# Optimization experiments

Measured on AMD Instinct MI355X. Metric: run time of the kernel, lower is better.

Reference implementation:

```python
import jax, jax.numpy as jnp
import numpy as np

N, D, H, E = 50000, 64, 4, 400000
LN_EPS = 1e-5


def setup_inputs() -> dict:
    key = jax.random.key(0)
    ks = jax.random.split(key, 8)
    x = jax.random.normal(ks[0], (N, D), dtype=jnp.float32)
    edge_index = jax.random.randint(ks[1], (2, E), 0, N, dtype=jnp.int64)
    # nn.Linear(dim, dim*heads, bias=False): weight shape (H*D, D)
    W_lin = jax.random.normal(ks[2], (H * D, D), dtype=jnp.float32) * (1.0 / np.sqrt(D))
    attn_src = jax.random.normal(ks[3], (H, D), dtype=jnp.float32) * 0.1
    attn_dst = jax.random.normal(ks[4], (H, D), dtype=jnp.float32) * 0.1
    # nn.Linear(dim*heads, dim): weight (D, H*D), bias (D,)
    W_out = jax.random.normal(ks[5], (D, H * D), dtype=jnp.float32) * (1.0 / np.sqrt(H * D))
    b_out = jnp.zeros((D,), dtype=jnp.float32)
    ln_g = jnp.ones((D,), dtype=jnp.float32)
    ln_b = jnp.zeros((D,), dtype=jnp.float32)
    return {"x": x, "edge_index": edge_index, "W_lin": W_lin,
            "attn_src": attn_src, "attn_dst": attn_dst,
            "W_out": W_out, "b_out": b_out, "ln_g": ln_g, "ln_b": ln_b}


def reference(x, edge_index, W_lin, attn_src, attn_dst, W_out, b_out, ln_g, ln_b):
    n = x.shape[0]
    i, j = edge_index[0], edge_index[1]  # dst, src node ids per edge
    xh = (x @ W_lin.T).reshape(n, H, D)                 # [N,H,D]
    # per-node attention contributions (equivalent to per-edge dot in source)
    s_dst = jnp.einsum('nhd,hd->nh', xh, attn_dst)      # [N,H]
    s_src = jnp.einsum('nhd,hd->nh', xh, attn_src)      # [N,H]
    alpha = jax.nn.leaky_relu(s_dst[i] + s_src[j], 0.2) # [E,H]
    alpha_exp = jnp.exp(alpha)                          # source uses raw exp (no max-shift)
    denom = jax.ops.segment_sum(alpha_exp, i, num_segments=n)  # [N,H]
    attn = alpha_exp / (denom[i] + 1e-9)                # [E,H]
    msg = attn[:, :, None] * xh[j]                      # [E,H,D]
    out = jax.ops.segment_sum(msg, i, num_segments=n)   # [N,H,D]
    out = out.reshape(n, H * D) @ W_out.T + b_out       # [N,D]
    y = jax.nn.elu(out) + x
    mu = jnp.mean(y, axis=-1, keepdims=True)
    var = jnp.mean(jnp.square(y - mu), axis=-1, keepdims=True)
    return (y - mu) * jax.lax.rsqrt(var + LN_EPS) * ln_g + ln_b
```

## Files before the change

kernel.cpp:

```cpp
#include <hip/hip_runtime.h>

#define N_NODES 50000
#define DIM     64
#define HEADS   4
#define NEDGES  400000
#define EHALF   200000
#define HD      256
#define MAXDEG  32
#define NPREP   200
#define ZSTRIDE 264

typedef _Float16 half2v __attribute__((ext_vector_type(2)));
typedef _Float16 half4v __attribute__((ext_vector_type(4)));
typedef _Float16 half8v __attribute__((ext_vector_type(8)));
typedef float    f32x4  __attribute__((ext_vector_type(4)));

union EU { int2 i2; half4v h; };

__global__ __launch_bounds__(256) void k_prep(
    const float* __restrict__ x,
    const float* __restrict__ W_lin,
    const float* __restrict__ attn_src,
    const float* __restrict__ attn_dst,
    const float* __restrict__ W_out,
    _Float16* __restrict__ G2T,
    _Float16* __restrict__ x16,
    float* __restrict__ S,
    int* __restrict__ cnt)
{
    __shared__ float weffsh[512];
    const int b = blockIdx.x, t = threadIdx.x;

    for (int id = t; id < 512; id += 256) {
        const int sd = id >> 8, rem = id & 255, h = rem >> 6, k = rem & 63;
        const float* av = sd ? attn_dst : attn_src;
        float acc = 0.f;
        for (int d = 0; d < DIM; ++d)
            acc = fmaf(av[h * DIM + d], W_lin[(h * DIM + d) * DIM + k], acc);
        weffsh[id] = acc;
    }

    for (int idx = b * 256 + t; idx < N_NODES; idx += NPREP * 256)
        cnt[idx] = 0;

    {
        const int id = b * 256 + t;
        if (id < 64 * 256) {
            const int d = id >> 8, rem = id & 255, m = rem >> 2, h = rem & 3;
            float acc = 0.f;
            for (int k = 0; k < DIM; ++k)
                acc = fmaf(W_lin[(h * DIM + k) * DIM + m],
                           W_out[d * HD + h * DIM + k], acc);
            G2T[d * HD + m * 4 + h] = (_Float16)acc;
        }
    }
    __syncthreads();

    for (int base = b * 32; base < N_NODES; base += NPREP * 32) {
        const int ni = base + (t >> 3);
        if (ni < N_NODES) {
            const int combo = t & 7;
            const float4* xr = (const float4*)(x + (size_t)ni * DIM);
            const float4* wr = (const float4*)(weffsh + combo * DIM);
            float acc = 0.f;
#pragma unroll
            for (int kp = 0; kp < 16; ++kp) {
                const float4 a = xr[kp], bw = wr[kp];
                acc = fmaf(a.x, bw.x, acc);
                acc = fmaf(a.y, bw.y, acc);
                acc = fmaf(a.z, bw.z, acc);
                acc = fmaf(a.w, bw.w, acc);
            }
            S[(size_t)ni * 8 + combo] = acc;
        }
        const size_t e0 = (size_t)base * DIM + (size_t)t * 8;
        if (e0 + 8 <= (size_t)N_NODES * DIM) {
            const float4 u = *(const float4*)(x + e0);
            const float4 v = *(const float4*)(x + e0 + 4);
            half8v hv;
            hv[0]=(_Float16)u.x; hv[1]=(_Float16)u.y; hv[2]=(_Float16)u.z; hv[3]=(_Float16)u.w;
            hv[4]=(_Float16)v.x; hv[5]=(_Float16)v.y; hv[6]=(_Float16)v.z; hv[7]=(_Float16)v.w;
            *(half8v*)(x16 + e0) = hv;
        }
    }
}

__global__ __launch_bounds__(256) void k_edge(
    const int* __restrict__ ei,
    const float* __restrict__ S,
    int* __restrict__ cnt,
    int4* __restrict__ bucketE)
{
    const int e = blockIdx.x * 256 + threadIdx.x;
    if (e >= EHALF) return;
    const int i0 = ei[e],         j0 = ei[NEDGES + e];
    const int i1 = ei[EHALF + e], j1 = ei[NEDGES + EHALF + e];
    const float4 sd0 = *(const float4*)(S + (size_t)i0 * 8 + 4);
    const float4 ss0 = *(const float4*)(S + (size_t)j0 * 8);
    const float4 sd1 = *(const float4*)(S + (size_t)i1 * 8 + 4);
    const float4 ss1 = *(const float4*)(S + (size_t)j1 * 8);
    float u;
    u = sd0.x + ss0.x; u = u > 0.f ? u : 0.2f * u; const float a0 = __expf(u);
    u = sd0.y + ss0.y; u = u > 0.f ? u : 0.2f * u; const float a1 = __expf(u);
    u = sd0.z + ss0.z; u = u > 0.f ? u : 0.2f * u; const float a2 = __expf(u);
    u = sd0.w + ss0.w; u = u > 0.f ? u : 0.2f * u; const float a3 = __expf(u);
    u = sd1.x + ss1.x; u = u > 0.f ? u : 0.2f * u; const float b0 = __expf(u);
    u = sd1.y + ss1.y; u = u > 0.f ? u : 0.2f * u; const float b1 = __expf(u);
    u = sd1.z + ss1.z; u = u > 0.f ? u : 0.2f * u; const float b2 = __expf(u);
    u = sd1.w + ss1.w; u = u > 0.f ? u : 0.2f * u; const float b3 = __expf(u);

    EU pk0; pk0.h[0]=(_Float16)a0; pk0.h[1]=(_Float16)a1;
            pk0.h[2]=(_Float16)a2; pk0.h[3]=(_Float16)a3;
    EU pk1; pk1.h[0]=(_Float16)b0; pk1.h[1]=(_Float16)b1;
            pk1.h[2]=(_Float16)b2; pk1.h[3]=(_Float16)b3;

    const int s0 = atomicAdd(&cnt[i0], 1);
    const int s1 = atomicAdd(&cnt[i1], 1);
    if (s0 < MAXDEG) {
        int4 ent; ent.x = j0; ent.y = pk0.i2.x; ent.z = pk0.i2.y; ent.w = 0;
        bucketE[(size_t)i0 * MAXDEG + s0] = ent;
    }
    if (s1 < MAXDEG) {
        int4 ent; ent.x = j1; ent.y = pk1.i2.x; ent.z = pk1.i2.y; ent.w = 0;
        bucketE[(size_t)i1 * MAXDEG + s1] = ent;
    }
}

__global__ __launch_bounds__(256) void k_ga(
    const int* __restrict__ cnt,
    const int4* __restrict__ bucketE,
    const _Float16* __restrict__ x16,
    const _Float16* __restrict__ G2T,
    const float* __restrict__ b_out,
    const float* __restrict__ ln_g,
    const float* __restrict__ ln_b,
    float* __restrict__ out)
{
    __shared__ _Float16 znsh[16 * ZSTRIDE];
    __shared__ float ysh[16][65];

    const int t = threadIdx.x, wv = t >> 6, l = t & 63;
    const int n0 = blockIdx.x * 16;
    const int side = l >> 5, p = l & 31;

    const int4 degv = *(const int4*)(cnt + n0 + wv * 4);
    int degc[4];
    degc[0] = degv.x < MAXDEG ? degv.x : MAXDEG;
    degc[1] = degv.y < MAXDEG ? degv.y : MAXDEG;
    degc[2] = degv.z < MAXDEG ? degv.z : MAXDEG;
    degc[3] = degv.w < MAXDEG ? degv.w : MAXDEG;
    int4 E[4];
#pragma unroll
    for (int r = 0; r < 4; ++r)
        E[r] = bucketE[(size_t)(n0 + wv * 4 + r) * MAXDEG + p];

    auto issue_group = [&](int r, int s, int deg, int* jjo, half2v* xvo) {
#pragma unroll
        for (int q = 0; q < 4; ++q) {
            const int ss = s + 2 * q + side;
            const int jv = __shfl(E[r].x, ss, 64);
            jjo[q] = (ss < deg) ? jv : 0;
        }
#pragma unroll
        for (int q = 0; q < 4; ++q)
            xvo[q] = *(const half2v*)(x16 + (size_t)jjo[q] * DIM + p * 2);
    };

    int jjc[4]; half2v xvc[4];
    issue_group(0, 0, degc[0], jjc, xvc);

#pragma unroll
    for (int r = 0; r < 4; ++r) {
        int jjn[4]; half2v xvn[4];
        if (r < 3) issue_group(r + 1, 0, degc[r + 1], jjn, xvn);

        float za[4] = {0.f, 0.f, 0.f, 0.f};
        float zb[4] = {0.f, 0.f, 0.f, 0.f};
        float dd[4] = {0.f, 0.f, 0.f, 0.f};

        auto consume_group = [&](int s, const half2v* xv) {
#pragma unroll
            for (int q = 0; q < 4; ++q) {
                const int ss = s + 2 * q + side;
                int ey = __shfl(E[r].y, ss, 64);
                int ez = __shfl(E[r].z, ss, 64);
                const bool v = ss < degc[r];
                ey = v ? ey : 0;
                ez = v ? ez : 0;
                EU u; u.i2 = make_int2(ey, ez);
                const float e0 = (float)u.h[0], e1 = (float)u.h[1];
                const float e2 = (float)u.h[2], e3 = (float)u.h[3];
                dd[0] += e0; dd[1] += e1; dd[2] += e2; dd[3] += e3;
                const float fa = (float)xv[q][0], fb = (float)xv[q][1];
                za[0] = fmaf(e0, fa, za[0]); za[1] = fmaf(e1, fa, za[1]);
                za[2] = fmaf(e2, fa, za[2]); za[3] = fmaf(e3, fa, za[3]);
                zb[0] = fmaf(e0, fb, zb[0]); zb[1] = fmaf(e1, fb, zb[1]);
                zb[2] = fmaf(e2, fb, zb[2]); zb[3] = fmaf(e3, fb, zb[3]);
            }
        };

        consume_group(0, xvc);
        for (int s = 8; s < degc[r]; s += 8) {
            int jr[4]; half2v xr[4];
            issue_group(r, s, degc[r], jr, xr);
            consume_group(s, xr);
        }

#pragma unroll
        for (int h = 0; h < 4; ++h) {
            dd[h] += __shfl_xor(dd[h], 32, 64);
            za[h] += __shfl_xor(za[h], 32, 64);
            zb[h] += __shfl_xor(zb[h], 32, 64);
        }
        const float r0 = 1.f / (dd[0] + 1e-9f), r1 = 1.f / (dd[1] + 1e-9f);
        const float r2 = 1.f / (dd[2] + 1e-9f), r3 = 1.f / (dd[3] + 1e-9f);
        if (side == 0) {
            half8v o;
            o[0] = (_Float16)(za[0] * r0); o[1] = (_Float16)(za[1] * r1);
            o[2] = (_Float16)(za[2] * r2); o[3] = (_Float16)(za[3] * r3);
            o[4] = (_Float16)(zb[0] * r0); o[5] = (_Float16)(zb[1] * r1);
            o[6] = (_Float16)(zb[2] * r2); o[7] = (_Float16)(zb[3] * r3);
            *(half8v*)(znsh + (wv * 4 + r) * ZSTRIDE + p * 8) = o;
        }

#pragma unroll
        for (int q = 0; q < 4; ++q) { jjc[q] = jjn[q]; xvc[q] = xvn[q]; }
    }
    __syncthreads();

    const int mrow = l & 15, quad = l >> 4;
    half8v A[8];
    const _Float16* zr = znsh + mrow * ZSTRIDE + quad * 8;
#pragma unroll
    for (int s = 0; s < 8; ++s)
        A[s] = *(const half8v*)(zr + 32 * s);

    const _Float16* gp = G2T + (size_t)(wv * 16 + mrow) * HD + quad * 8;
    f32x4 c = {0.f, 0.f, 0.f, 0.f};
#pragma unroll
    for (int s = 0; s < 8; ++s)
        c = __builtin_amdgcn_mfma_f32_16x16x32_f16(A[s], *(const half8v*)(gp + 32 * s), c, 0, 0, 0);

    const int col = wv * 16 + mrow;
    const float bo = b_out[col];
#pragma unroll
    for (int rho = 0; rho < 4; ++rho) {
        const int nl = quad * 4 + rho;
        const float o = c[rho] + bo;
        const float eo = o > 0.f ? o : expm1f(o);
        ysh[nl][col] = eo + (float)x16[(size_t)(n0 + nl) * DIM + col];
    }
    __syncthreads();

    const float g = ln_g[l], bb = ln_b[l];
#pragma unroll
    for (int r = 0; r < 4; ++r) {
        const int nl = wv * 4 + r;
        const float y = ysh[nl][l];
        float sum = y;
#pragma unroll
        for (int off = 32; off > 0; off >>= 1) sum += __shfl_xor(sum, off, 64);
        const float mu = sum * (1.f / 64.f);
        const float dy = y - mu;
        float vs = dy * dy;
#pragma unroll
        for (int off = 32; off > 0; off >>= 1) vs += __shfl_xor(vs, off, 64);
        const float rr = rsqrtf(vs * (1.f / 64.f) + 1e-5f);
        out[(size_t)(n0 + nl) * DIM + l] = dy * rr * g + bb;
    }
}

extern "C" void kernel_launch(void* const* d_in, const int* in_sizes, int n_in,
                              void* d_out, int out_size, void* d_ws, size_t ws_size,
                              hipStream_t stream)
{
    const float* x        = (const float*)d_in[0];
    const int*   ei       = (const int*)d_in[1];
    const float* W_lin    = (const float*)d_in[2];
    const float* attn_src = (const float*)d_in[3];
    const float* attn_dst = (const float*)d_in[4];
    const float* W_out    = (const float*)d_in[5];
    const float* b_out    = (const float*)d_in[6];
    const float* ln_g     = (const float*)d_in[7];
    const float* ln_b     = (const float*)d_in[8];
    float* out = (float*)d_out;

    char* ws = (char*)d_ws;
    _Float16* x16    = (_Float16*)ws;
    float*    S      = (float*)(x16 + (size_t)N_NODES * DIM);
    _Float16* G2T    = (_Float16*)(S + (size_t)N_NODES * 8);
    int*      cnt    = (int*)(G2T + 64 * HD);
    int4*     bucketE= (int4*)(cnt + N_NODES);

    k_prep<<<NPREP, 256, 0, stream>>>(x, W_lin, attn_src, attn_dst, W_out,
                                      G2T, x16, S, cnt);

    k_edge<<<(EHALF + 255) / 256, 256, 0, stream>>>(ei, S, cnt, bucketE);

    k_ga<<<N_NODES / 16, 256, 0, stream>>>(cnt, bucketE, x16, G2T,
                                           b_out, ln_g, ln_b, out);
}
```

Measured before the change: 160.8 us.

## Fuse edge bucketing into prep and compute attention weights in gather kernel

Removes the separate edge kernel. Edge bucketing now happens inside k_prep through atomic slot claims, and it stores only source indices, 4 bytes per slot instead of a 16-byte int4. The gather kernel now reads S for the source and destination nodes and computes the leaky-relu/exp weights itself, and cnt is zeroed with hipMemsetAsync. This saves a launch and bucket bandwidth, at the cost of extra S gathers in k_ga and heavier atomic work inside the prep kernel.

```diff
diff --git a/kernel.cpp b/kernel.cpp
--- a/kernel.cpp
+++ b/kernel.cpp
@@ -4,10 +4,9 @@
 #define DIM     64
 #define HEADS   4
 #define NEDGES  400000
-#define EHALF   200000
 #define HD      256
 #define MAXDEG  32
-#define NPREP   200
+#define NPREP   256
 #define ZSTRIDE 264
 
 typedef _Float16 half2v __attribute__((ext_vector_type(2)));
@@ -23,13 +22,22 @@
     const float* __restrict__ attn_src,
     const float* __restrict__ attn_dst,
     const float* __restrict__ W_out,
+    const int* __restrict__ ei,
     _Float16* __restrict__ G2T,
     _Float16* __restrict__ x16,
     float* __restrict__ S,
-    int* __restrict__ cnt)
+    int* __restrict__ cnt,
+    int* __restrict__ bucketJ)
 {
     __shared__ float weffsh[512];
     const int b = blockIdx.x, t = threadIdx.x;
+
+    for (int e = b * 256 + t; e < NEDGES; e += NPREP * 256) {
+        const int i = ei[e];
+        const int j = ei[NEDGES + e];
+        const int slot = atomicAdd(&cnt[i], 1);
+        if (slot < MAXDEG) bucketJ[(size_t)i * MAXDEG + slot] = j;
+    }
 
     for (int id = t; id < 512; id += 256) {
         const int sd = id >> 8, rem = id & 255, h = rem >> 6, k = rem & 63;
@@ -39,9 +47,6 @@
             acc = fmaf(av[h * DIM + d], W_lin[(h * DIM + d) * DIM + k], acc);
         weffsh[id] = acc;
     }
-
-    for (int idx = b * 256 + t; idx < N_NODES; idx += NPREP * 256)
-        cnt[idx] = 0;
 
     {
         const int id = b * 256 + t;
@@ -85,50 +90,10 @@
     }
 }
 
-__global__ __launch_bounds__(256) void k_edge(
-    const int* __restrict__ ei,
-    const float* __restrict__ S,
-    int* __restrict__ cnt,
-    int4* __restrict__ bucketE)
-{
-    const int e = blockIdx.x * 256 + threadIdx.x;
-    if (e >= EHALF) return;
-    const int i0 = ei[e],         j0 = ei[NEDGES + e];
-    const int i1 = ei[EHALF + e], j1 = ei[NEDGES + EHALF + e];
-    const float4 sd0 = *(const float4*)(S + (size_t)i0 * 8 + 4);
-    const float4 ss0 = *(const float4*)(S + (size_t)j0 * 8);
-    const float4 sd1 = *(const float4*)(S + (size_t)i1 * 8 + 4);
-    const float4 ss1 = *(const float4*)(S + (size_t)j1 * 8);
-    float u;
-    u = sd0.x + ss0.x; u = u > 0.f ? u : 0.2f * u; const float a0 = __expf(u);
-    u = sd0.y + ss0.y; u = u > 0.f ? u : 0.2f * u; const float a1 = __expf(u);
-    u = sd0.z + ss0.z; u = u > 0.f ? u : 0.2f * u; const float a2 = __expf(u);
-    u = sd0.w + ss0.w; u = u > 0.f ? u : 0.2f * u; const float a3 = __expf(u);
-    u = sd1.x + ss1.x; u = u > 0.f ? u : 0.2f * u; const float b0 = __expf(u);
-    u = sd1.y + ss1.y; u = u > 0.f ? u : 0.2f * u; const float b1 = __expf(u);
-    u = sd1.z + ss1.z; u = u > 0.f ? u : 0.2f * u; const float b2 = __expf(u);
-    u = sd1.w + ss1.w; u = u > 0.f ? u : 0.2f * u; const float b3 = __expf(u);
-
-    EU pk0; pk0.h[0]=(_Float16)a0; pk0.h[1]=(_Float16)a1;
-            pk0.h[2]=(_Float16)a2; pk0.h[3]=(_Float16)a3;
-    EU pk1; pk1.h[0]=(_Float16)b0; pk1.h[1]=(_Float16)b1;
-            pk1.h[2]=(_Float16)b2; pk1.h[3]=(_Float16)b3;
-
-    const int s0 = atomicAdd(&cnt[i0], 1);
-    const int s1 = atomicAdd(&cnt[i1], 1);
-    if (s0 < MAXDEG) {
-        int4 ent; ent.x = j0; ent.y = pk0.i2.x; ent.z = pk0.i2.y; ent.w = 0;
-        bucketE[(size_t)i0 * MAXDEG + s0] = ent;
-    }
-    if (s1 < MAXDEG) {
-        int4 ent; ent.x = j1; ent.y = pk1.i2.x; ent.z = pk1.i2.y; ent.w = 0;
-        bucketE[(size_t)i1 * MAXDEG + s1] = ent;
-    }
-}
-
 __global__ __launch_bounds__(256) void k_ga(
     const int* __restrict__ cnt,
-    const int4* __restrict__ bucketE,
+    const int* __restrict__ bucketJ,
+    const float* __restrict__ S,
     const _Float16* __restrict__ x16,
     const _Float16* __restrict__ G2T,
     const float* __restrict__ b_out,
@@ -149,16 +114,42 @@
     degc[1] = degv.y < MAXDEG ? degv.y : MAXDEG;
     degc[2] = degv.z < MAXDEG ? degv.z : MAXDEG;
     degc[3] = degv.w < MAXDEG ? degv.w : MAXDEG;
-    int4 E[4];
-#pragma unroll
-    for (int r = 0; r < 4; ++r)
-        E[r] = bucketE[(size_t)(n0 + wv * 4 + r) * MAXDEG + p];
+
+    int Jr[4];
+#pragma unroll
+    for (int r = 0; r < 4; ++r)
+        Jr[r] = bucketJ[(size_t)(n0 + wv * 4 + r) * MAXDEG + p];
+#pragma unroll
+    for (int r = 0; r < 4; ++r)
+        Jr[r] = (p < degc[r]) ? Jr[r] : 0;
+
+    float4 SSr[4], SDr[4];
+#pragma unroll
+    for (int r = 0; r < 4; ++r)
+        SSr[r] = *(const float4*)(S + (size_t)Jr[r] * 8);
+#pragma unroll
+    for (int r = 0; r < 4; ++r)
+        SDr[r] = *(const float4*)(S + (size_t)(n0 + wv * 4 + r) * 8 + 4);
+
+    int Ey[4], Ez[4];
+#pragma unroll
+    for (int r = 0; r < 4; ++r) {
+        float u;
+        u = SDr[r].x + SSr[r].x; u = u > 0.f ? u : 0.2f * u; const float e0 = __expf(u);
+        u = SDr[r].y + SSr[r].y; u = u > 0.f ? u : 0.2f * u; const float e1 = __expf(u);
+        u = SDr[r].z + SSr[r].z; u = u > 0.f ? u : 0.2f * u; const float e2 = __expf(u);
+        u = SDr[r].w + SSr[r].w; u = u > 0.f ? u : 0.2f * u; const float e3 = __expf(u);
+        EU pk;
+        pk.h[0] = (_Float16)e0; pk.h[1] = (_Float16)e1;
+        pk.h[2] = (_Float16)e2; pk.h[3] = (_Float16)e3;
+        Ey[r] = pk.i2.x; Ez[r] = pk.i2.y;
+    }
 
     auto issue_group = [&](int r, int s, int deg, int* jjo, half2v* xvo) {
 #pragma unroll
         for (int q = 0; q < 4; ++q) {
             const int ss = s + 2 * q + side;
-            const int jv = __shfl(E[r].x, ss, 64);
+            const int jv = __shfl(Jr[r], ss, 64);
             jjo[q] = (ss < deg) ? jv : 0;
         }
 #pragma unroll
@@ -182,8 +173,8 @@
 #pragma unroll
             for (int q = 0; q < 4; ++q) {
                 const int ss = s + 2 * q + side;
-                int ey = __shfl(E[r].y, ss, 64);
-                int ez = __shfl(E[r].z, ss, 64);
+                int ey = __shfl(Ey[r], ss, 64);
+                int ez = __shfl(Ez[r], ss, 64);
                 const bool v = ss < degc[r];
                 ey = v ? ey : 0;
                 ez = v ? ez : 0;
@@ -201,9 +192,9 @@
 
         consume_group(0, xvc);
         for (int s = 8; s < degc[r]; s += 8) {
-            int jr[4]; half2v xr[4];
-            issue_group(r, s, degc[r], jr, xr);
-            consume_group(s, xr);
+            int jr2[4]; half2v xr2[4];
+            issue_group(r, s, degc[r], jr2, xr2);
+            consume_group(s, xr2);
         }
 
 #pragma unroll
@@ -290,13 +281,13 @@
     float*    S      = (float*)(x16 + (size_t)N_NODES * DIM);
     _Float16* G2T    = (_Float16*)(S + (size_t)N_NODES * 8);
     int*      cnt    = (int*)(G2T + 64 * HD);
-    int4*     bucketE= (int4*)(cnt + N_NODES);
-
-    k_prep<<<NPREP, 256, 0, stream>>>(x, W_lin, attn_src, attn_dst, W_out,
-                                      G2T, x16, S, cnt);
-
-    k_edge<<<(EHALF + 255) / 256, 256, 0, stream>>>(ei, S, cnt, bucketE);
-
-    k_ga<<<N_NODES / 16, 256, 0, stream>>>(cnt, bucketE, x16, G2T,
+    int*      bucketJ= cnt + N_NODES;
+
+    hipMemsetAsync(cnt, 0, (size_t)N_NODES * sizeof(int), stream);
+
+    k_prep<<<NPREP, 256, 0, stream>>>(x, W_lin, attn_src, attn_dst, W_out, ei,
+                                      G2T, x16, S, cnt, bucketJ);
+
+    k_ga<<<N_NODES / 16, 256, 0, stream>>>(cnt, bucketJ, S, x16, G2T,
                                            b_out, ln_g, ln_b, out);
 }
```

New measurement: 155.8 us (median of 2 runs). 3.1% less time.
